# Kernel optimization log

Measured on AMD Instinct MI355X. Metric: run time of the kernel, lower is better.

## Reference

```python
import jax, jax.numpy as jnp
import numpy as np

HIDDEN = 1024
NUM_HEADS = 16
HEAD_DIM = HIDDEN // NUM_HEADS
ROPE_THETA = 10000.0


def rope_tables(seq_len, head_dim, theta):
    inv_freq = 1.0 / theta ** (jnp.arange(0, head_dim, 2, dtype=jnp.float32) / head_dim)
    pos = jnp.arange(seq_len, dtype=jnp.float32)
    freqs = jnp.outer(pos, inv_freq)  # [S, hd/2]
    return jnp.cos(freqs), jnp.sin(freqs)


def apply_rope(x, cos, sin):
    # x: [B, nh, S, hd]; cos/sin: [S, hd/2]
    x1, x2 = jnp.split(x, 2, axis=-1)
    return jnp.concatenate([x1 * cos - x2 * sin, x2 * cos + x1 * sin], axis=-1)


def setup_inputs() -> dict:
    key = jax.random.key(0)
    k1, k2, k3 = jax.random.split(key, 3)
    B, S = 2, 2048
    hidden_states = jax.random.normal(k1, (B, S, HIDDEN), dtype=jnp.float32)
    # nn.Linear stores weight as [out, in]; y = x @ W.T
    Wqkv = jax.random.normal(k2, (3 * HIDDEN, HIDDEN), dtype=jnp.float32) * (HIDDEN ** -0.5)
    Wo = jax.random.normal(k3, (HIDDEN, HIDDEN), dtype=jnp.float32) * (HIDDEN ** -0.5)
    return {"hidden_states": hidden_states, "Wqkv": Wqkv, "Wo": Wo}


def reference(hidden_states, Wqkv, Wo):
    B, S, H = hidden_states.shape
    qkv = hidden_states @ Wqkv.T  # [B, S, 3H]
    qkv = qkv.reshape(B, S, 3, NUM_HEADS, HEAD_DIM)
    q, k, v = jnp.moveaxis(qkv, 2, 0)  # each [B, S, nh, hd]
    q = jnp.transpose(q, (0, 2, 1, 3))  # [B, nh, S, hd]
    k = jnp.transpose(k, (0, 2, 1, 3))
    v = jnp.transpose(v, (0, 2, 1, 3))
    cos, sin = rope_tables(S, HEAD_DIM, ROPE_THETA)
    q = apply_rope(q, cos, sin)
    k = apply_rope(k, cos, sin)
    scale = 1.0 / jnp.sqrt(jnp.asarray(HEAD_DIM, dtype=q.dtype))
    scores = jnp.einsum("bhqd,bhkd->bhqk", q, k) * scale
    causal = jnp.tril(jnp.ones((S, S), dtype=bool))
    scores = jnp.where(causal, scores, jnp.finfo(scores.dtype).min)
    attn = jax.nn.softmax(scores, axis=-1)
    out = jnp.einsum("bhqk,bhkd->bhqd", attn, v)  # [B, nh, S, hd]
    out = jnp.transpose(out, (0, 2, 1, 3)).reshape(B, S, H)
    return out @ Wo.T
```

## Files before the change

### kernel.cpp

```cpp
#include <hip/hip_runtime.h>
#include <hip/hip_bf16.h>
#include <math.h>

typedef __bf16 bf16_t;
typedef __attribute__((ext_vector_type(8))) __bf16 bf16x8;
typedef __attribute__((ext_vector_type(4))) float f32x4;
typedef __attribute__((ext_vector_type(16))) float f32x16;
typedef __attribute__((ext_vector_type(4))) unsigned u32x4;

#define AS1(p) ((__attribute__((address_space(1))) void*)(p))
#define AS3(p) ((__attribute__((address_space(3))) void*)(p))

__device__ inline void cvt8(const float* __restrict__ in, bf16_t* __restrict__ out, int i) {
  const float4* p = (const float4*)in;
  float4 a = p[2 * i], b = p[2 * i + 1];
  bf16x8 o;
  o[0] = (bf16_t)a.x; o[1] = (bf16_t)a.y; o[2] = (bf16_t)a.z; o[3] = (bf16_t)a.w;
  o[4] = (bf16_t)b.x; o[5] = (bf16_t)b.y; o[6] = (bf16_t)b.z; o[7] = (bf16_t)b.w;
  ((bf16x8*)out)[i] = o;
}

__global__ __launch_bounds__(256)
void prep_all(const float* __restrict__ hid, const float* __restrict__ wqkv,
              const float* __restrict__ wo, bf16_t* __restrict__ hidb,
              bf16_t* __restrict__ wqkvb, bf16_t* __restrict__ wob,
              float* __restrict__ cosb, float* __restrict__ sinb) {
  const int bid = blockIdx.x, tid = threadIdx.x;
  if (bid < 2048) {
    cvt8(hid, hidb, bid * 256 + tid);
  } else if (bid < 3584) {
    cvt8(wqkv, wqkvb, (bid - 2048) * 256 + tid);
  } else if (bid < 4096) {
    cvt8(wo, wob, (bid - 3584) * 256 + tid);
  } else {
    int t = (bid - 4096) * 256 + tid;
    int s = t >> 5, i = t & 31;
    float inv = powf(10000.0f, -(float)i / 32.0f);
    float sv, cv;
    sincosf((float)s * inv, &sv, &cv);
    cosb[t] = cv;
    sinb[t] = sv;
  }
}

__global__ __launch_bounds__(256)
void pack_rope(bf16_t* __restrict__ qkv, const float* __restrict__ cosb,
               const float* __restrict__ sinb, bf16_t* __restrict__ Kp) {
  __shared__ bf16_t vl[64][72];
  const int t = blockIdx.x, bh = blockIdx.y, b = bh >> 4, h = bh & 15;
  const int tid = threadIdx.x;
  const int r = tid >> 2, j = tid & 3;
  const int s = t * 64 + r;
  bf16_t* base = qkv + ((size_t)(b * 2048 + s)) * 3072 + h * 64;
  const float* cb = cosb + s * 32 + j * 8;
  const float* sb = sinb + s * 32 + j * 8;
  bf16x8 q1 = *(const bf16x8*)(base + j * 8);
  bf16x8 q2 = *(const bf16x8*)(base + j * 8 + 32);
  bf16x8 k1 = *(const bf16x8*)(base + 1024 + j * 8);
  bf16x8 k2 = *(const bf16x8*)(base + 1024 + j * 8 + 32);
  bf16x8 v1 = *(const bf16x8*)(base + 2048 + j * 8);
  bf16x8 v2 = *(const bf16x8*)(base + 2048 + j * 8 + 32);
  const float QS = 0.125f * 1.4426950408889634f;
  bf16x8 qo1, qo2, ko1, ko2;
#pragma unroll
  for (int i = 0; i < 8; ++i) {
    float c = cb[i], sn = sb[i];
    float a1 = (float)q1[i], a2 = (float)q2[i];
    qo1[i] = (bf16_t)((a1 * c - a2 * sn) * QS);
    qo2[i] = (bf16_t)((a2 * c + a1 * sn) * QS);
    float b1 = (float)k1[i], b2 = (float)k2[i];
    ko1[i] = (bf16_t)(b1 * c - b2 * sn);
    ko2[i] = (bf16_t)(b2 * c + b1 * sn);
  }
  *(bf16x8*)(base + j * 8) = qo1;
  *(bf16x8*)(base + j * 8 + 32) = qo2;
  bf16_t* kd = Kp + ((size_t)(bh * 32 + t)) * 4096 + r * 64;
  *(bf16x8*)(kd + ((j ^ (r & 7)) * 8)) = ko1;
  *(bf16x8*)(kd + (((j + 4) ^ (r & 7)) * 8)) = ko2;
#pragma unroll
  for (int i = 0; i < 8; ++i) { vl[r][j * 8 + i] = v1[i]; vl[r][j * 8 + 32 + i] = v2[i]; }
  __syncthreads();
  const int d = r;
  bf16x8 o1, o2;
#pragma unroll
  for (int i = 0; i < 8; ++i) { o1[i] = vl[j * 16 + i][d]; o2[i] = vl[j * 16 + 8 + i][d]; }
  bf16_t* vd = base + 2048;
  *(bf16x8*)(vd + (((2 * j) ^ (d & 7)) * 8)) = o1;
  *(bf16x8*)(vd + (((2 * j + 1) ^ (d & 7)) * 8)) = o2;
}

template <typename OutT>
__global__ __launch_bounds__(256, 2)
void gemm_nt(const bf16_t* __restrict__ A, const bf16_t* __restrict__ B,
             OutT* __restrict__ C, int M, int N, int K) {
  __shared__ __align__(16) bf16_t lA[128 * 64];
  __shared__ __align__(16) bf16_t lB[128 * 64];
  const int tid = threadIdx.x;
  const int wid = tid >> 6, lane = tid & 63;
  const int lr = lane & 15, lg = lane >> 4;
  const int nwg = gridDim.x * gridDim.y;
  int lin = blockIdx.y * gridDim.x + blockIdx.x;
  lin = (lin & 7) * (nwg >> 3) + (lin >> 3);
  const int m0 = (lin / gridDim.x) * 128, n0 = (lin % gridDim.x) * 128;
  const int wm = (wid >> 1) * 64, wn = (wid & 1) * 64;
  const int srow = lane >> 3;
  const int scol = (lane & 7) * 8;
  f32x4 acc[4][4];
#pragma unroll
  for (int i = 0; i < 4; ++i)
#pragma unroll
    for (int j = 0; j < 4; ++j) acc[i][j] = f32x4{0.f, 0.f, 0.f, 0.f};

  const int nk = K >> 6;
  for (int kt = 0; kt < nk; ++kt) {
    const int k0 = kt << 6;
    __syncthreads();
#pragma unroll
    for (int i = 0; i < 4; ++i) {
      int c = (wid << 2) + i;
      int r = (c << 3) + srow;
      __builtin_amdgcn_global_load_lds(AS1(A + (size_t)(m0 + r) * K + k0 + scol),
                                       AS3(&lA[c * 512]), 16, 0, 0);
      __builtin_amdgcn_global_load_lds(AS1(B + (size_t)(n0 + r) * K + k0 + scol),
                                       AS3(&lB[c * 512]), 16, 0, 0);
    }
    __syncthreads();
#pragma unroll
    for (int ks = 0; ks < 2; ++ks) {
      bf16x8 af[4], bfr[4];
#pragma unroll
      for (int i = 0; i < 4; ++i) {
        af[i]  = *(const bf16x8*)&lA[(wm + i * 16 + lr) * 64 + ks * 32 + lg * 8];
        bfr[i] = *(const bf16x8*)&lB[(wn + i * 16 + lr) * 64 + ks * 32 + lg * 8];
      }
#pragma unroll
      for (int i = 0; i < 4; ++i)
#pragma unroll
        for (int j = 0; j < 4; ++j)
          acc[i][j] = __builtin_amdgcn_mfma_f32_16x16x32_bf16(af[i], bfr[j], acc[i][j], 0, 0, 0);
    }
  }
#pragma unroll
  for (int i = 0; i < 4; ++i)
#pragma unroll
    for (int j = 0; j < 4; ++j)
#pragma unroll
      for (int r = 0; r < 4; ++r) {
        int row = m0 + wm + i * 16 + lg * 4 + r;
        int col = n0 + wn + j * 16 + lr;
        C[(size_t)row * N + col] = (OutT)acc[i][j][r];
      }
}

__device__ inline unsigned pkbf(float a, float b) {
  bf16_t x = (bf16_t)a, y = (bf16_t)b;
  return (unsigned)__builtin_bit_cast(unsigned short, x) |
         ((unsigned)__builtin_bit_cast(unsigned short, y) << 16);
}
__device__ inline f32x16 zero16() {
  f32x16 z;
#pragma unroll
  for (int r = 0; r < 16; ++r) z[r] = 0.f;
  return z;
}

__device__ const unsigned char ROLE_LUT[44] = {
    19, 18, 17, 16,
    15, 95, 159, 158,
    14, 94, 93, 157,
    13, 92, 156, 91, 155, 154,
    12, 90, 89, 153, 152,
    11, 88, 87, 151, 150,
    10, 86, 85, 149, 148,
    9, 84,
    8, 7, 6, 5, 4, 3, 2, 1, 0};

__global__ __launch_bounds__(128, 2)
void attn_fwd(const bf16_t* __restrict__ qkv, const bf16_t* __restrict__ Kp,
              bf16_t* __restrict__ O, bf16_t* __restrict__ Po, float* __restrict__ Plp) {
  __shared__ __align__(16) bf16_t Ksh[2][4096];
  __shared__ __align__(16) bf16_t Vsh[2][4096];
  const int tid = threadIdx.x, wid = tid >> 6, lane = tid & 63;
  const int ln = lane & 31, h = lane >> 5;
  const int lin = blockIdx.x;
  const int e = ROLE_LUT[lin >> 5];
  const int bh = lin & 31;
  const int c = e & 31, kind = e >> 6;
  const int b = bh >> 4, hd = bh & 15;
  const int t0 = (kind == 2) ? ((c + 1) >> 1) : 0;
  const int t1 = (kind == 1) ? ((c + 1) >> 1) : c + 1;
  const int qw = c * 64 + wid * 32;

  const bf16_t* Qrow = qkv + ((size_t)(b * 2048 + qw + ln)) * 3072 + hd * 64;
  bf16x8 qf[4];
#pragma unroll
  for (int t = 0; t < 4; ++t) qf[t] = *(const bf16x8*)(Qrow + t * 16 + h * 8);

  f32x16 o0 = zero16(), o1 = zero16();
  float lp = 0.f;

  const bf16_t* Kbase = Kp + ((size_t)bh * 32) * 4096 + tid * 8;
  const bf16_t* Vbase = qkv + ((size_t)(b * 2048 + (tid >> 3))) * 3072 + 2048 + hd * 64 + (tid & 7) * 8;

#define STAGE(T, BUF)                                                                     \
  do {                                                                                    \
    const bf16_t* ks = Kbase + (size_t)(T) * 4096;                                        \
    __builtin_amdgcn_global_load_lds(AS1(ks),        AS3(&Ksh[BUF][tid * 8]), 16, 0, 0);  \
    __builtin_amdgcn_global_load_lds(AS1(ks + 1024), AS3(&Ksh[BUF][1024 + tid * 8]), 16, 0, 0); \
    __builtin_amdgcn_global_load_lds(AS1(ks + 2048), AS3(&Ksh[BUF][2048 + tid * 8]), 16, 0, 0); \
    __builtin_amdgcn_global_load_lds(AS1(ks + 3072), AS3(&Ksh[BUF][3072 + tid * 8]), 16, 0, 0); \
    const bf16_t* vs = Vbase + (size_t)(T) * 64 * 3072;                                   \
    __builtin_amdgcn_global_load_lds(AS1(vs),             AS3(&Vsh[BUF][tid * 8]), 16, 0, 0);        \
    __builtin_amdgcn_global_load_lds(AS1(vs + 16 * 3072), AS3(&Vsh[BUF][1024 + tid * 8]), 16, 0, 0); \
    __builtin_amdgcn_global_load_lds(AS1(vs + 32 * 3072), AS3(&Vsh[BUF][2048 + tid * 8]), 16, 0, 0); \
    __builtin_amdgcn_global_load_lds(AS1(vs + 48 * 3072), AS3(&Vsh[BUF][3072 + tid * 8]), 16, 0, 0); \
  } while (0)

  STAGE(t0, t0 & 1);
  for (int t = t0; t < t1; ++t) {
    asm volatile("s_waitcnt vmcnt(0)" ::: "memory");
    __builtin_amdgcn_s_barrier();
    if (t + 1 < t1) STAGE(t + 1, (t + 1) & 1);
    const bf16_t* K = &Ksh[t & 1][0];
    const bf16_t* V = &Vsh[t & 1][0];
    f32x16 s0 = zero16(), s1 = zero16();
    __builtin_amdgcn_s_setprio(1);
#pragma unroll
    for (int u = 0; u < 4; ++u) {
      const int ch = 2 * u + h;
      bf16x8 k0 = *(const bf16x8*)&K[ln * 64 + ((ch ^ (ln & 7)) * 8)];
      bf16x8 k1 = *(const bf16x8*)&K[(32 + ln) * 64 + ((ch ^ (ln & 7)) * 8)];
      s0 = __builtin_amdgcn_mfma_f32_32x32x16_bf16(k0, qf[u], s0, 0, 0, 0);
      s1 = __builtin_amdgcn_mfma_f32_32x32x16_bf16(k1, qf[u], s1, 0, 0, 0);
    }
    __builtin_amdgcn_s_setprio(0);
    if (t == c) {
      const int qg = qw + ln, k0g = t * 64;
#pragma unroll
      for (int r = 0; r < 16; ++r) {
        int kv = k0g + (r & 3) + 8 * (r >> 2) + 4 * h;
        if (kv > qg) s0[r] = -3e38f;
        if (kv + 32 > qg) s1[r] = -3e38f;
      }
    }
#pragma unroll
    for (int r = 0; r < 16; ++r) {
      float p0 = __builtin_amdgcn_exp2f(s0[r]); lp += p0; s0[r] = p0;
      float p1 = __builtin_amdgcn_exp2f(s1[r]); lp += p1; s1[r] = p1;
    }
    __builtin_amdgcn_s_setprio(1);
#pragma unroll
    for (int u = 0; u < 4; ++u) {
      const int w = u & 1;
      f32x16 sv = (u >> 1) ? s1 : s0;
      unsigned x  = pkbf(sv[8 * w + 0], sv[8 * w + 1]);
      unsigned x2 = pkbf(sv[8 * w + 2], sv[8 * w + 3]);
      unsigned y  = pkbf(sv[8 * w + 4], sv[8 * w + 5]);
      unsigned y2 = pkbf(sv[8 * w + 6], sv[8 * w + 7]);
      asm volatile("v_permlane32_swap_b32 %0, %1" : "+v"(x), "+v"(y));
      asm volatile("v_permlane32_swap_b32 %0, %1" : "+v"(x2), "+v"(y2));
      u32x4 pw; pw[0] = x; pw[1] = x2; pw[2] = y; pw[3] = y2;
      bf16x8 pf = __builtin_bit_cast(bf16x8, pw);
      const int ch = 2 * u + h;
      bf16x8 v0 = *(const bf16x8*)&V[ln * 64 + ((ch ^ (ln & 7)) * 8)];
      bf16x8 v1 = *(const bf16x8*)&V[(32 + ln) * 64 + ((ch ^ (ln & 7)) * 8)];
      o0 = __builtin_amdgcn_mfma_f32_32x32x16_bf16(v0, pf, o0, 0, 0, 0);
      o1 = __builtin_amdgcn_mfma_f32_32x32x16_bf16(v1, pf, o1, 0, 0, 0);
    }
    __builtin_amdgcn_s_setprio(0);
  }
#undef STAGE
  float lpf = lp + __shfl_xor(lp, 32, 64);
  if (kind == 0) {
    float inv = 1.0f / lpf;
    bf16_t* Oaddr = O + ((size_t)(b * 2048 + qw + ln)) * 1024 + hd * 64;
#pragma unroll
    for (int D = 0; D < 2; ++D) {
      f32x16 ov = D ? o1 : o0;
#pragma unroll
      for (int Q = 0; Q < 4; ++Q) {
        uint2 w;
        w.x = pkbf(ov[4 * Q + 0] * inv, ov[4 * Q + 1] * inv);
        w.y = pkbf(ov[4 * Q + 2] * inv, ov[4 * Q + 3] * inv);
        *(uint2*)(Oaddr + D * 32 + Q * 8 + 4 * h) = w;
      }
    }
  } else {
    const int slot = (bh * 12 + (c - 20)) * 2 + (kind - 1);
    const int qi = wid * 32 + ln;
    if (h == 0) Plp[slot * 64 + qi] = lpf;
    bf16_t* Paddr = Po + ((size_t)(slot * 64 + qi)) * 64;
#pragma unroll
    for (int D = 0; D < 2; ++D) {
      f32x16 ov = D ? o1 : o0;
#pragma unroll
      for (int Q = 0; Q < 4; ++Q) {
        uint2 w;
        w.x = pkbf(ov[4 * Q + 0], ov[4 * Q + 1]);
        w.y = pkbf(ov[4 * Q + 2], ov[4 * Q + 3]);
        *(uint2*)(Paddr + D * 32 + Q * 8 + 4 * h) = w;
      }
    }
  }
}

__global__ __launch_bounds__(64)
void attn_combine(const bf16_t* __restrict__ Po, const float* __restrict__ Plp,
                  bf16_t* __restrict__ O) {
  const int blk = blockIdx.x;
  const int bh = blk / 12, sc = blk % 12;
  const int b = bh >> 4, hd = bh & 15;
  const int c = 20 + sc;
  const int q = threadIdx.x;
  const int slotA = (bh * 12 + sc) * 2, slotB = slotA + 1;
  float inv = 1.0f / (Plp[slotA * 64 + q] + Plp[slotB * 64 + q]);
  const bf16x8* pa = (const bf16x8*)(Po + ((size_t)(slotA * 64 + q)) * 64);
  const bf16x8* pb = (const bf16x8*)(Po + ((size_t)(slotB * 64 + q)) * 64);
  bf16_t* oaddr = O + ((size_t)(b * 2048 + c * 64 + q)) * 1024 + hd * 64;
#pragma unroll
  for (int j = 0; j < 8; ++j) {
    bf16x8 a = pa[j], v = pb[j];
    bf16x8 w;
#pragma unroll
    for (int k = 0; k < 8; ++k) w[k] = (bf16_t)(((float)a[k] + (float)v[k]) * inv);
    ((bf16x8*)oaddr)[j] = w;
  }
}

extern "C" void kernel_launch(void* const* d_in, const int* in_sizes, int n_in,
                              void* d_out, int out_size, void* d_ws, size_t ws_size,
                              hipStream_t stream) {
  const float* hid  = (const float*)d_in[0];
  const float* wqkv = (const float*)d_in[1];
  const float* wo   = (const float*)d_in[2];
  float* out = (float*)d_out;
  char* ws = (char*)d_ws;
  bf16_t* hidb  = (bf16_t*)(ws);
  bf16_t* wqkvb = (bf16_t*)(ws + 8388608);
  bf16_t* wob   = (bf16_t*)(ws + 14680064);
  bf16_t* qkvb  = (bf16_t*)(ws + 16777216);
  float*  cosb  = (float*)(ws + 41943040);
  float*  sinb  = (float*)(ws + 42205184);
  bf16_t* Ob    = (bf16_t*)(ws + 42467328);
  bf16_t* Kp    = (bf16_t*)(ws);
  bf16_t* Po    = (bf16_t*)(ws + 8388608);
  float*  Plp   = (float*)(ws + 41943040);

  prep_all<<<4352, 256, 0, stream>>>(hid, wqkv, wo, hidb, wqkvb, wob, cosb, sinb);
  gemm_nt<bf16_t><<<dim3(24, 32), 256, 0, stream>>>(hidb, wqkvb, qkvb, 4096, 3072, 1024);
  pack_rope<<<dim3(32, 32), 256, 0, stream>>>(qkvb, cosb, sinb, Kp);
  attn_fwd<<<1408, 128, 0, stream>>>(qkvb, Kp, Ob, Po, Plp);
  attn_combine<<<384, 64, 0, stream>>>(Po, Plp, Ob);
  gemm_nt<float><<<dim3(8, 32), 256, 0, stream>>>(Ob, wob, out, 4096, 1024, 1024);
}
```

Before: 118.9 us.

## Pre-pack V into MFMA fragment order and load it straight to registers

A new pack_v kernel transposes V and writes it into the now-unused K columns of the qkv buffer, already in MFMA operand order. The attention kernel then reads each lane's V fragments directly from global memory into registers instead of staging V through shared memory. This halves the LDS footprint, and the occupancy hint is raised from 2 to 4 blocks per CU. The softmax row-sum is split across four accumulators to shorten the dependency chain. The costs are an extra kernel launch and V global-load latency now sitting inside the loop instead of being prefetched a tile ahead.

```diff
diff --git a/kernel.cpp b/kernel.cpp
--- a/kernel.cpp
+++ b/kernel.cpp
@@ -46,7 +46,6 @@
 __global__ __launch_bounds__(256)
 void pack_rope(bf16_t* __restrict__ qkv, const float* __restrict__ cosb,
                const float* __restrict__ sinb, bf16_t* __restrict__ Kp) {
-  __shared__ bf16_t vl[64][72];
   const int t = blockIdx.x, bh = blockIdx.y, b = bh >> 4, h = bh & 15;
   const int tid = threadIdx.x;
   const int r = tid >> 2, j = tid & 3;
@@ -58,8 +57,6 @@
   bf16x8 q2 = *(const bf16x8*)(base + j * 8 + 32);
   bf16x8 k1 = *(const bf16x8*)(base + 1024 + j * 8);
   bf16x8 k2 = *(const bf16x8*)(base + 1024 + j * 8 + 32);
-  bf16x8 v1 = *(const bf16x8*)(base + 2048 + j * 8);
-  bf16x8 v2 = *(const bf16x8*)(base + 2048 + j * 8 + 32);
   const float QS = 0.125f * 1.4426950408889634f;
   bf16x8 qo1, qo2, ko1, ko2;
 #pragma unroll
@@ -77,16 +74,29 @@
   bf16_t* kd = Kp + ((size_t)(bh * 32 + t)) * 4096 + r * 64;
   *(bf16x8*)(kd + ((j ^ (r & 7)) * 8)) = ko1;
   *(bf16x8*)(kd + (((j + 4) ^ (r & 7)) * 8)) = ko2;
+}
+
+__global__ __launch_bounds__(256)
+void pack_v(bf16_t* __restrict__ qkv) {
+  __shared__ bf16_t vl[64][72];
+  const int t = blockIdx.x, bh = blockIdx.y, b = bh >> 4, hd = bh & 15;
+  const int tid = threadIdx.x;
+  const int r = tid >> 2, j = tid & 3;
+  const bf16_t* vsrc = qkv + ((size_t)(b * 2048 + t * 64 + r)) * 3072 + 2048 + hd * 64;
+  bf16x8 v1 = *(const bf16x8*)(vsrc + j * 8);
+  bf16x8 v2 = *(const bf16x8*)(vsrc + j * 8 + 32);
 #pragma unroll
   for (int i = 0; i < 8; ++i) { vl[r][j * 8 + i] = v1[i]; vl[r][j * 8 + 32 + i] = v2[i]; }
   __syncthreads();
-  const int d = r;
-  bf16x8 o1, o2;
-#pragma unroll
-  for (int i = 0; i < 8; ++i) { o1[i] = vl[j * 16 + i][d]; o2[i] = vl[j * 16 + 8 + i][d]; }
-  bf16_t* vd = base + 2048;
-  *(bf16x8*)(vd + (((2 * j) ^ (d & 7)) * 8)) = o1;
-  *(bf16x8*)(vd + (((2 * j + 1) ^ (d & 7)) * 8)) = o2;
+  const int g = tid >> 5, l0 = tid & 31;
+  const int d = (g < 4) ? l0 : (32 + l0);
+  const int ch0 = 2 * (g & 3);
+  bf16x8 f0, f1;
+#pragma unroll
+  for (int i = 0; i < 8; ++i) { f0[i] = vl[8 * ch0 + i][d]; f1[i] = vl[8 * ch0 + 8 + i][d]; }
+  bf16_t* dst = qkv + ((size_t)(b * 2048 + t * 64 + hd * 4 + (g >> 1))) * 3072 + 1024 + (g & 1) * 512;
+  *(bf16x8*)(dst + l0 * 8) = f0;
+  *(bf16x8*)(dst + (l0 + 32) * 8) = f1;
 }
 
 template <typename OutT>
@@ -175,11 +185,10 @@
     9, 84,
     8, 7, 6, 5, 4, 3, 2, 1, 0};
 
-__global__ __launch_bounds__(128, 2)
+__global__ __launch_bounds__(128, 4)
 void attn_fwd(const bf16_t* __restrict__ qkv, const bf16_t* __restrict__ Kp,
               bf16_t* __restrict__ O, bf16_t* __restrict__ Po, float* __restrict__ Plp) {
   __shared__ __align__(16) bf16_t Ksh[2][4096];
-  __shared__ __align__(16) bf16_t Vsh[2][4096];
   const int tid = threadIdx.x, wid = tid >> 6, lane = tid & 63;
   const int ln = lane & 31, h = lane >> 5;
   const int lin = blockIdx.x;
@@ -197,32 +206,31 @@
   for (int t = 0; t < 4; ++t) qf[t] = *(const bf16x8*)(Qrow + t * 16 + h * 8);
 
   f32x16 o0 = zero16(), o1 = zero16();
-  float lp = 0.f;
+  float lpa = 0.f, lpb = 0.f, lpc = 0.f, lpd = 0.f;
 
   const bf16_t* Kbase = Kp + ((size_t)bh * 32) * 4096 + tid * 8;
-  const bf16_t* Vbase = qkv + ((size_t)(b * 2048 + (tid >> 3))) * 3072 + 2048 + hd * 64 + (tid & 7) * 8;
-
-#define STAGE(T, BUF)                                                                     \
+  const bf16_t* Vp0 = qkv + ((size_t)(b * 2048 + hd * 4)) * 3072 + 1024 + lane * 8;
+
+#define KSTAGE(T, BUF)                                                                    \
   do {                                                                                    \
     const bf16_t* ks = Kbase + (size_t)(T) * 4096;                                        \
     __builtin_amdgcn_global_load_lds(AS1(ks),        AS3(&Ksh[BUF][tid * 8]), 16, 0, 0);  \
     __builtin_amdgcn_global_load_lds(AS1(ks + 1024), AS3(&Ksh[BUF][1024 + tid * 8]), 16, 0, 0); \
     __builtin_amdgcn_global_load_lds(AS1(ks + 2048), AS3(&Ksh[BUF][2048 + tid * 8]), 16, 0, 0); \
     __builtin_amdgcn_global_load_lds(AS1(ks + 3072), AS3(&Ksh[BUF][3072 + tid * 8]), 16, 0, 0); \
-    const bf16_t* vs = Vbase + (size_t)(T) * 64 * 3072;                                   \
-    __builtin_amdgcn_global_load_lds(AS1(vs),             AS3(&Vsh[BUF][tid * 8]), 16, 0, 0);        \
-    __builtin_amdgcn_global_load_lds(AS1(vs + 16 * 3072), AS3(&Vsh[BUF][1024 + tid * 8]), 16, 0, 0); \
-    __builtin_amdgcn_global_load_lds(AS1(vs + 32 * 3072), AS3(&Vsh[BUF][2048 + tid * 8]), 16, 0, 0); \
-    __builtin_amdgcn_global_load_lds(AS1(vs + 48 * 3072), AS3(&Vsh[BUF][3072 + tid * 8]), 16, 0, 0); \
   } while (0)
 
-  STAGE(t0, t0 & 1);
+  KSTAGE(t0, t0 & 1);
   for (int t = t0; t < t1; ++t) {
     asm volatile("s_waitcnt vmcnt(0)" ::: "memory");
     __builtin_amdgcn_s_barrier();
-    if (t + 1 < t1) STAGE(t + 1, (t + 1) & 1);
+    if (t + 1 < t1) KSTAGE(t + 1, (t + 1) & 1);
+    const bf16_t* vb = Vp0 + (size_t)t * (64 * 3072);
+    bf16x8 v0[4];
+#pragma unroll
+    for (int u = 0; u < 4; ++u)
+      v0[u] = *(const bf16x8*)(vb + (u >> 1) * 3072 + (u & 1) * 512);
     const bf16_t* K = &Ksh[t & 1][0];
-    const bf16_t* V = &Vsh[t & 1][0];
     f32x16 s0 = zero16(), s1 = zero16();
     __builtin_amdgcn_s_setprio(1);
 #pragma unroll
@@ -234,6 +242,10 @@
       s1 = __builtin_amdgcn_mfma_f32_32x32x16_bf16(k1, qf[u], s1, 0, 0, 0);
     }
     __builtin_amdgcn_s_setprio(0);
+    bf16x8 v1[4];
+#pragma unroll
+    for (int u = 0; u < 4; ++u)
+      v1[u] = *(const bf16x8*)(vb + (2 + (u >> 1)) * 3072 + (u & 1) * 512);
     if (t == c) {
       const int qg = qw + ln, k0g = t * 64;
 #pragma unroll
@@ -244,9 +256,15 @@
       }
     }
 #pragma unroll
-    for (int r = 0; r < 16; ++r) {
-      float p0 = __builtin_amdgcn_exp2f(s0[r]); lp += p0; s0[r] = p0;
-      float p1 = __builtin_amdgcn_exp2f(s1[r]); lp += p1; s1[r] = p1;
+    for (int r = 0; r < 16; r += 4) {
+      float p0 = __builtin_amdgcn_exp2f(s0[r]);     lpa += p0; s0[r] = p0;
+      float p1 = __builtin_amdgcn_exp2f(s0[r + 1]); lpb += p1; s0[r + 1] = p1;
+      float p2 = __builtin_amdgcn_exp2f(s0[r + 2]); lpc += p2; s0[r + 2] = p2;
+      float p3 = __builtin_amdgcn_exp2f(s0[r + 3]); lpd += p3; s0[r + 3] = p3;
+      float p4 = __builtin_amdgcn_exp2f(s1[r]);     lpa += p4; s1[r] = p4;
+      float p5 = __builtin_amdgcn_exp2f(s1[r + 1]); lpb += p5; s1[r + 1] = p5;
+      float p6 = __builtin_amdgcn_exp2f(s1[r + 2]); lpc += p6; s1[r + 2] = p6;
+      float p7 = __builtin_amdgcn_exp2f(s1[r + 3]); lpd += p7; s1[r + 3] = p7;
     }
     __builtin_amdgcn_s_setprio(1);
 #pragma unroll
@@ -261,15 +279,13 @@
       asm volatile("v_permlane32_swap_b32 %0, %1" : "+v"(x2), "+v"(y2));
       u32x4 pw; pw[0] = x; pw[1] = x2; pw[2] = y; pw[3] = y2;
       bf16x8 pf = __builtin_bit_cast(bf16x8, pw);
-      const int ch = 2 * u + h;
-      bf16x8 v0 = *(const bf16x8*)&V[ln * 64 + ((ch ^ (ln & 7)) * 8)];
-      bf16x8 v1 = *(const bf16x8*)&V[(32 + ln) * 64 + ((ch ^ (ln & 7)) * 8)];
-      o0 = __builtin_amdgcn_mfma_f32_32x32x16_bf16(v0, pf, o0, 0, 0, 0);
-      o1 = __builtin_amdgcn_mfma_f32_32x32x16_bf16(v1, pf, o1, 0, 0, 0);
+      o0 = __builtin_amdgcn_mfma_f32_32x32x16_bf16(v0[u], pf, o0, 0, 0, 0);
+      o1 = __builtin_amdgcn_mfma_f32_32x32x16_bf16(v1[u], pf, o1, 0, 0, 0);
     }
     __builtin_amdgcn_s_setprio(0);
   }
-#undef STAGE
+#undef KSTAGE
+  float lp = (lpa + lpb) + (lpc + lpd);
   float lpf = lp + __shfl_xor(lp, 32, 64);
   if (kind == 0) {
     float inv = 1.0f / lpf;
@@ -349,6 +365,7 @@
   prep_all<<<4352, 256, 0, stream>>>(hid, wqkv, wo, hidb, wqkvb, wob, cosb, sinb);
   gemm_nt<bf16_t><<<dim3(24, 32), 256, 0, stream>>>(hidb, wqkvb, qkvb, 4096, 3072, 1024);
   pack_rope<<<dim3(32, 32), 256, 0, stream>>>(qkvb, cosb, sinb, Kp);
+  pack_v<<<dim3(32, 32), 256, 0, stream>>>(qkvb);
   attn_fwd<<<1408, 128, 0, stream>>>(qkvb, Kp, Ob, Po, Plp);
   attn_combine<<<384, 64, 0, stream>>>(Po, Plp, Ob);
   gemm_nt<float><<<dim3(8, 32), 256, 0, stream>>>(Ob, wob, out, 4096, 1024, 1024);
```

New measurement: 120.3 us. Within noise of the previous version (+1.2%).

## Fuse RoPE, Q scaling and K/V repacking into QKV GEMM epilogue

Applied to the files above, without the earlier changes.

The QKV projection GEMM now applies RoPE and the softmax scale to Q, writes rotated K directly into the swizzled packed K buffer, and writes V transposed in its swizzled layout from the accumulators. This removes the separate pack_rope kernel launch and its extra read/write pass over the QKV buffer. In exchange the epilogue performs scattered 2-byte stores and per-element cos/sin loads, which may coalesce poorly. Workspace offsets for Kp/Po/Plp are moved so they no longer alias the inputs still being read.

```diff
diff --git a/kernel.cpp b/kernel.cpp
--- a/kernel.cpp
+++ b/kernel.cpp
@@ -10,6 +10,18 @@
 
 #define AS1(p) ((__attribute__((address_space(1))) void*)(p))
 #define AS3(p) ((__attribute__((address_space(3))) void*)(p))
+
+__device__ inline unsigned pkbf(float a, float b) {
+  bf16_t x = (bf16_t)a, y = (bf16_t)b;
+  return (unsigned)__builtin_bit_cast(unsigned short, x) |
+         ((unsigned)__builtin_bit_cast(unsigned short, y) << 16);
+}
+__device__ inline f32x16 zero16() {
+  f32x16 z;
+#pragma unroll
+  for (int r = 0; r < 16; ++r) z[r] = 0.f;
+  return z;
+}
 
 __device__ inline void cvt8(const float* __restrict__ in, bf16_t* __restrict__ out, int i) {
   const float4* p = (const float4*)in;
@@ -43,56 +55,110 @@
   }
 }
 
-__global__ __launch_bounds__(256)
-void pack_rope(bf16_t* __restrict__ qkv, const float* __restrict__ cosb,
-               const float* __restrict__ sinb, bf16_t* __restrict__ Kp) {
-  __shared__ bf16_t vl[64][72];
-  const int t = blockIdx.x, bh = blockIdx.y, b = bh >> 4, h = bh & 15;
+__global__ __launch_bounds__(256, 2)
+void gemm_qkv(const bf16_t* __restrict__ A, const bf16_t* __restrict__ B,
+              bf16_t* __restrict__ qkv, bf16_t* __restrict__ Kp,
+              const float* __restrict__ cosb, const float* __restrict__ sinb) {
+  __shared__ __align__(16) bf16_t lA[128 * 64];
+  __shared__ __align__(16) bf16_t lB[128 * 64];
+  const int K = 1024;
   const int tid = threadIdx.x;
-  const int r = tid >> 2, j = tid & 3;
-  const int s = t * 64 + r;
-  bf16_t* base = qkv + ((size_t)(b * 2048 + s)) * 3072 + h * 64;
-  const float* cb = cosb + s * 32 + j * 8;
-  const float* sb = sinb + s * 32 + j * 8;
-  bf16x8 q1 = *(const bf16x8*)(base + j * 8);
-  bf16x8 q2 = *(const bf16x8*)(base + j * 8 + 32);
-  bf16x8 k1 = *(const bf16x8*)(base + 1024 + j * 8);
-  bf16x8 k2 = *(const bf16x8*)(base + 1024 + j * 8 + 32);
-  bf16x8 v1 = *(const bf16x8*)(base + 2048 + j * 8);
-  bf16x8 v2 = *(const bf16x8*)(base + 2048 + j * 8 + 32);
-  const float QS = 0.125f * 1.4426950408889634f;
-  bf16x8 qo1, qo2, ko1, ko2;
-#pragma unroll
-  for (int i = 0; i < 8; ++i) {
-    float c = cb[i], sn = sb[i];
-    float a1 = (float)q1[i], a2 = (float)q2[i];
-    qo1[i] = (bf16_t)((a1 * c - a2 * sn) * QS);
-    qo2[i] = (bf16_t)((a2 * c + a1 * sn) * QS);
-    float b1 = (float)k1[i], b2 = (float)k2[i];
-    ko1[i] = (bf16_t)(b1 * c - b2 * sn);
-    ko2[i] = (bf16_t)(b2 * c + b1 * sn);
-  }
-  *(bf16x8*)(base + j * 8) = qo1;
-  *(bf16x8*)(base + j * 8 + 32) = qo2;
-  bf16_t* kd = Kp + ((size_t)(bh * 32 + t)) * 4096 + r * 64;
-  *(bf16x8*)(kd + ((j ^ (r & 7)) * 8)) = ko1;
-  *(bf16x8*)(kd + (((j + 4) ^ (r & 7)) * 8)) = ko2;
-#pragma unroll
-  for (int i = 0; i < 8; ++i) { vl[r][j * 8 + i] = v1[i]; vl[r][j * 8 + 32 + i] = v2[i]; }
-  __syncthreads();
-  const int d = r;
-  bf16x8 o1, o2;
-#pragma unroll
-  for (int i = 0; i < 8; ++i) { o1[i] = vl[j * 16 + i][d]; o2[i] = vl[j * 16 + 8 + i][d]; }
-  bf16_t* vd = base + 2048;
-  *(bf16x8*)(vd + (((2 * j) ^ (d & 7)) * 8)) = o1;
-  *(bf16x8*)(vd + (((2 * j + 1) ^ (d & 7)) * 8)) = o2;
-}
-
-template <typename OutT>
+  const int wid = tid >> 6, lane = tid & 63;
+  const int lr = lane & 15, lg = lane >> 4;
+  const int nwg = gridDim.x * gridDim.y;
+  int lin = blockIdx.y * gridDim.x + blockIdx.x;
+  lin = (lin & 7) * (nwg >> 3) + (lin >> 3);
+  const int m0 = (lin / gridDim.x) * 128, n0 = (lin % gridDim.x) * 128;
+  const int wm = (wid >> 1) * 64, wn = (wid & 1) * 64;
+  const int srow = lane >> 3;
+  const int scol = (lane & 7) * 8;
+  f32x4 acc[4][4];
+#pragma unroll
+  for (int i = 0; i < 4; ++i)
+#pragma unroll
+    for (int j = 0; j < 4; ++j) acc[i][j] = f32x4{0.f, 0.f, 0.f, 0.f};
+
+  for (int kt = 0; kt < 16; ++kt) {
+    const int k0 = kt << 6;
+    __syncthreads();
+#pragma unroll
+    for (int i = 0; i < 4; ++i) {
+      int c = (wid << 2) + i;
+      int r = (c << 3) + srow;
+      __builtin_amdgcn_global_load_lds(AS1(A + (size_t)(m0 + r) * K + k0 + scol),
+                                       AS3(&lA[c * 512]), 16, 0, 0);
+      __builtin_amdgcn_global_load_lds(AS1(B + (size_t)(n0 + r) * K + k0 + scol),
+                                       AS3(&lB[c * 512]), 16, 0, 0);
+    }
+    __syncthreads();
+#pragma unroll
+    for (int ks = 0; ks < 2; ++ks) {
+      bf16x8 af[4], bfr[4];
+#pragma unroll
+      for (int i = 0; i < 4; ++i) {
+        af[i]  = *(const bf16x8*)&lA[(wm + i * 16 + lr) * 64 + ks * 32 + lg * 8];
+        bfr[i] = *(const bf16x8*)&lB[(wn + i * 16 + lr) * 64 + ks * 32 + lg * 8];
+      }
+#pragma unroll
+      for (int i = 0; i < 4; ++i)
+#pragma unroll
+        for (int j = 0; j < 4; ++j)
+          acc[i][j] = __builtin_amdgcn_mfma_f32_16x16x32_bf16(af[i], bfr[j], acc[i][j], 0, 0, 0);
+    }
+  }
+  const int sec = n0 >> 10;
+  const int hcol = ((n0 + wn) & 1023) >> 6;
+  if (sec == 2) {
+#pragma unroll
+    for (int i = 0; i < 4; ++i) {
+      int token0 = m0 + wm + i * 16 + lg * 4;
+      int bb = token0 >> 11;
+      int t = (token0 & 2047) >> 6;
+      int kv0 = token0 & 63;
+      bf16_t* vd = qkv + ((size_t)(bb * 2048 + t * 64)) * 3072 + 2048 + hcol * 64;
+#pragma unroll
+      for (int j = 0; j < 4; ++j) {
+        int d = j * 16 + lr;
+        uint2 w;
+        w.x = pkbf(acc[i][j][0], acc[i][j][1]);
+        w.y = pkbf(acc[i][j][2], acc[i][j][3]);
+        *(uint2*)(vd + (size_t)d * 3072 + (((kv0 >> 3) ^ (d & 7)) * 8) + (kv0 & 7)) = w;
+      }
+    }
+  } else {
+    const float SC = sec ? 1.0f : 0.125f * 1.4426950408889634f;
+#pragma unroll
+    for (int i = 0; i < 4; ++i)
+#pragma unroll
+      for (int r = 0; r < 4; ++r) {
+        int token = m0 + wm + i * 16 + lg * 4 + r;
+        int s = token & 2047;
+#pragma unroll
+        for (int j = 0; j < 2; ++j) {
+          int f = j * 16 + lr;
+          float cv = cosb[s * 32 + f], sv = sinb[s * 32 + f];
+          float x1 = acc[i][j][r], x2 = acc[i][j + 2][r];
+          float y1 = (x1 * cv - x2 * sv) * SC;
+          float y2 = (x2 * cv + x1 * sv) * SC;
+          if (sec == 0) {
+            bf16_t* qd = qkv + (size_t)token * 3072 + hcol * 64;
+            qd[f] = (bf16_t)y1;
+            qd[f + 32] = (bf16_t)y2;
+          } else {
+            int bb = token >> 11, t = (token & 2047) >> 6, rk = token & 63;
+            bf16_t* kd = Kp + ((size_t)((bb * 16 + hcol) * 32 + t)) * 4096 + rk * 64;
+            int c1 = f >> 3;
+            kd[((c1 ^ (rk & 7)) * 8) + (lr & 7)] = (bf16_t)y1;
+            kd[(((c1 + 4) ^ (rk & 7)) * 8) + (lr & 7)] = (bf16_t)y2;
+          }
+        }
+      }
+  }
+}
+
 __global__ __launch_bounds__(256, 2)
-void gemm_nt(const bf16_t* __restrict__ A, const bf16_t* __restrict__ B,
-             OutT* __restrict__ C, int M, int N, int K) {
+void gemm_nt_f32(const bf16_t* __restrict__ A, const bf16_t* __restrict__ B,
+                 float* __restrict__ C, int M, int N, int K) {
   __shared__ __align__(16) bf16_t lA[128 * 64];
   __shared__ __align__(16) bf16_t lB[128 * 64];
   const int tid = threadIdx.x;
@@ -148,20 +214,8 @@
       for (int r = 0; r < 4; ++r) {
         int row = m0 + wm + i * 16 + lg * 4 + r;
         int col = n0 + wn + j * 16 + lr;
-        C[(size_t)row * N + col] = (OutT)acc[i][j][r];
-      }
-}
-
-__device__ inline unsigned pkbf(float a, float b) {
-  bf16_t x = (bf16_t)a, y = (bf16_t)b;
-  return (unsigned)__builtin_bit_cast(unsigned short, x) |
-         ((unsigned)__builtin_bit_cast(unsigned short, y) << 16);
-}
-__device__ inline f32x16 zero16() {
-  f32x16 z;
-#pragma unroll
-  for (int r = 0; r < 16; ++r) z[r] = 0.f;
-  return z;
+        C[(size_t)row * N + col] = acc[i][j][r];
+      }
 }
 
 __device__ const unsigned char ROLE_LUT[44] = {
@@ -342,14 +396,13 @@
   float*  cosb  = (float*)(ws + 41943040);
   float*  sinb  = (float*)(ws + 42205184);
   bf16_t* Ob    = (bf16_t*)(ws + 42467328);
-  bf16_t* Kp    = (bf16_t*)(ws);
-  bf16_t* Po    = (bf16_t*)(ws + 8388608);
-  float*  Plp   = (float*)(ws + 41943040);
+  bf16_t* Kp    = (bf16_t*)(ws + 52428800);
+  bf16_t* Po    = (bf16_t*)(ws + 60817408);
+  float*  Plp   = (float*)(ws + 67108864);
 
   prep_all<<<4352, 256, 0, stream>>>(hid, wqkv, wo, hidb, wqkvb, wob, cosb, sinb);
-  gemm_nt<bf16_t><<<dim3(24, 32), 256, 0, stream>>>(hidb, wqkvb, qkvb, 4096, 3072, 1024);
-  pack_rope<<<dim3(32, 32), 256, 0, stream>>>(qkvb, cosb, sinb, Kp);
+  gemm_qkv<<<dim3(24, 32), 256, 0, stream>>>(hidb, wqkvb, qkvb, Kp, cosb, sinb);
   attn_fwd<<<1408, 128, 0, stream>>>(qkvb, Kp, Ob, Po, Plp);
   attn_combine<<<384, 64, 0, stream>>>(Po, Plp, Ob);
-  gemm_nt<float><<<dim3(8, 32), 256, 0, stream>>>(Ob, wob, out, 4096, 1024, 1024);
-}
+  gemm_nt_f32<<<dim3(8, 32), 256, 0, stream>>>(Ob, wob, out, 4096, 1024, 1024);
+}
```

After: 115.1 us. 3.2% less time.
